# Kernel tuning notes

Measured on AMD Instinct MI355X. Metric: run time of the kernel, lower is better.

## Reference

```python
import jax, jax.numpy as jnp
import numpy as np
from jax.scipy.special import logsumexp

NODES = 128
K = 8
N = 4096  # num data samples; must equal M (original code stacks (N,) with (M,))
Z = NODES * (NODES - 1) // 2


def setup_inputs() -> dict:
    key = jax.random.key(0)
    k1, k2, k3 = jax.random.split(key, 3)
    X = jax.random.normal(k1, (N, NODES), dtype=jnp.float32)
    noise = jax.random.normal(k2, (N, NODES), dtype=jnp.float32)
    theta = jax.random.normal(k3, (K, 2, Z), dtype=jnp.float32)
    logc = jnp.zeros((K,), dtype=jnp.float32)
    return {"X": X, "noise": noise, "theta": theta, "logc": logc}


def reference(X, noise, theta, logc):
    n = X.shape[0]
    m = noise.shape[0]
    nodes = X.shape[1]
    iu, ju = np.triu_indices(nodes, k=1)  # static pair indices, z = nodes*(nodes-1)//2

    def mixture_logprob(A):
        # A: (S, nodes) -> per-component log prob summed over all node pairs, then
        # logsumexp over the K mixture components with weights logc.
        d = A[:, iu] - A[:, ju]                      # (S, z) pairwise phase diffs
        lp = (jnp.einsum('kz,sz->ks', theta[:, 0], jnp.cos(d))
              + jnp.einsum('kz,sz->ks', theta[:, 1], jnp.sin(d)))  # (K, S)
        return logsumexp(lp + logc[:, None], axis=0)  # (S,)

    lp_data = mixture_logprob(X)      # (n,)
    lp_noise = mixture_logprob(noise)  # (m,) == (n,)

    logN = jnp.log(jnp.float32(n))
    logM = jnp.log(jnp.float32(m))
    # log_nx = log_ny = 0 in the original code
    log_J1_denom = jnp.logaddexp(logN + lp_data, logM)
    log_J2_denom = jnp.logaddexp(logN + lp_noise, logM)
    J = (jnp.mean(logN + lp_data - log_J1_denom)
         + jnp.mean(logN - log_J2_denom))
    return J
```

## Files before the change

kernel.cpp:

```cpp
#include <hip/hip_runtime.h>
#include <hip/hip_bf16.h>
#include <math.h>

#define NODES 128
#define KMIX  8
#define NSAMP 4096
#define STOT  8192
#define ZPAIR 8128
#define FDIM  256

using bf16x8 = __attribute__((ext_vector_type(8))) short;
using f32x4  = __attribute__((ext_vector_type(4))) float;

#define OF_F   ((size_t)0)
#define OF_M   (OF_F + (size_t)STOT * FDIM / 2)
#define OF_LP4 (OF_M + (size_t)KMIX * FDIM * FDIM / 2)
#define OF_PT  (OF_LP4 + (size_t)4 * KMIX * STOT)
#define OF_CT  (OF_PT + 32)

#define VMC(N) asm volatile("s_waitcnt vmcnt(" #N ")" ::: "memory")
#define LGKM0  asm volatile("s_waitcnt lgkmcnt(0)" ::: "memory")
#define SBAR   asm volatile("s_barrier" ::: "memory")

__device__ __forceinline__ float bf2f(short u) {
    union { unsigned u32; float f; } cv;
    cv.u32 = ((unsigned)(unsigned short)u) << 16;
    return cv.f;
}
__device__ __forceinline__ short f2bf(float f) {
    union { float f; unsigned u32; } cv; cv.f = f;
    unsigned r = cv.u32 + 0x7fff + ((cv.u32 >> 16) & 1);
    return (short)(r >> 16);
}
__device__ __forceinline__ float softplusf(float x) {
    return fmaxf(x, 0.0f) + log1pf(expf(-fabsf(x)));
}

#define FEAT_BLOCKS (STOT * NODES / 256)
#define WB_BLOCKS   (KMIX * FDIM * FDIM / 256)

__global__ void prep_kernel(const float* __restrict__ X, const float* __restrict__ noise,
                            const float* __restrict__ theta,
                            short* __restrict__ F, short* __restrict__ W,
                            unsigned* __restrict__ ctr) {
    const int b = blockIdx.x, t = threadIdx.x;
    if (b == 0 && t == 0) *ctr = 0u;
    if (b < FEAT_BLOCKS) {
        int idx = b * 256 + t;
        int s = idx >> 7, i = idx & 127;
        float v = (s < NSAMP) ? X[idx] : noise[idx - NSAMP * NODES];
        float sv, cv;
        __sincosf(v, &sv, &cv);
        F[(size_t)s * FDIM + i]       = f2bf(cv);
        F[(size_t)s * FDIM + 128 + i] = f2bf(sv);
    } else {
        int idx = (b - FEAT_BLOCKS) * 256 + t;
        int j = idx & 255, i = (idx >> 8) & 255, k = idx >> 16;
        int a = i & 127, bb = j & 127;
        int hi = i >> 7, hj = j >> 7;
        float val = 0.0f;
        if (a != bb) {
            int p = a < bb ? a : bb;
            int q = a < bb ? bb : a;
            int z = p * 127 - (p * (p - 1)) / 2 + (q - p - 1);
            if (hi == hj) {
                val = 0.5f * theta[(size_t)(k * 2 + 0) * ZPAIR + z];
            } else if (hi == 1 && hj == 0) {
                float t1 = theta[(size_t)(k * 2 + 1) * ZPAIR + z];
                val = (a < bb) ? t1 : -t1;
            }
        }
        W[idx] = f2bf(val);
    }
}

__global__ __launch_bounds__(256, 2) void gemm_fused(
        const short* __restrict__ F, const short* __restrict__ M,
        float* __restrict__ lp2) {
    __shared__ short Ft[2][128 * 64];
    __shared__ short Mt[2][128 * 64];

    const int bid = blockIdx.x;
    const int k   = bid >> 6;
    const int st  = bid & 63;
    const int sbase = st * 128;

    const int t = threadIdx.x;
    const int wid = t >> 6, lane = t & 63;
    const int wm = wid >> 1, wn = wid & 1;

    const short* Mk = M + (size_t)k * FDIM * FDIM;

    const int rg = lane >> 3;
    const int sc = (lane & 7) ^ rg;

    f32x4 acc0[4][4] = {};
    f32x4 acc1[4][4] = {};

    auto stageF = [&](int buf, int c) {
        #pragma unroll
        for (int q = 0; q < 4; q++) {
            int g = wid * 4 + q;
            const short* src = F + ((size_t)(sbase + g * 8 + rg)) * FDIM + c * 64 + sc * 8;
            __builtin_amdgcn_global_load_lds((const unsigned*)src,
                                             (unsigned*)&Ft[buf][g * 512], 16, 0, 0);
        }
    };
    auto stageW = [&](int buf, int ihrow, int c) {
        #pragma unroll
        for (int q = 0; q < 4; q++) {
            int g = wid * 4 + q;
            const short* src = Mk + ((size_t)(ihrow * 128 + g * 8 + rg)) * FDIM + c * 64 + sc * 8;
            __builtin_amdgcn_global_load_lds((const unsigned*)src,
                                             (unsigned*)&Mt[buf][g * 512], 16, 0, 0);
        }
    };

    const int rlow = lane & 15, kq = lane >> 4;

    bf16x8 afr[4][2], bfr[4][2];
    auto loadA = [&](int fbuf) {
        #pragma unroll
        for (int m = 0; m < 4; m++) {
            int row = wm * 64 + m * 16 + rlow;
            #pragma unroll
            for (int kk = 0; kk < 2; kk++) {
                int c16 = (kk * 4 + kq) ^ (row & 7);
                afr[m][kk] = *(const bf16x8*)&Ft[fbuf][row * 64 + c16 * 8];
            }
        }
    };
    auto loadB = [&](int mbuf) {
        #pragma unroll
        for (int n = 0; n < 4; n++) {
            int row = wn * 64 + n * 16 + rlow;
            #pragma unroll
            for (int kk = 0; kk < 2; kk++) {
                int c16 = (kk * 4 + kq) ^ (row & 7);
                bfr[n][kk] = *(const bf16x8*)&Mt[mbuf][row * 64 + c16 * 8];
            }
        }
    };
    auto mfma = [&](f32x4 (&acc)[4][4]) {
        #pragma unroll
        for (int m = 0; m < 4; m++)
            #pragma unroll
            for (int n = 0; n < 4; n++)
                #pragma unroll
                for (int kk = 0; kk < 2; kk++)
                    acc[m][n] = __builtin_amdgcn_mfma_f32_16x16x32_bf16(
                        afr[m][kk], bfr[n][kk], acc[m][n], 0, 0, 0);
    };

    stageF(0, 0); stageW(0, 0, 0); stageW(1, 1, 0);

    VMC(4); SBAR;
    loadA(0); loadB(0);
    LGKM0; SBAR;
    stageF(1, 1); stageW(0, 0, 1);
    mfma(acc0);
    VMC(8); SBAR;
    loadA(0); loadB(1);
    LGKM0; SBAR;
    stageW(1, 1, 1);
    mfma(acc1);
    VMC(4); SBAR;
    loadA(1); loadB(0);
    LGKM0; SBAR;
    stageF(0, 2); stageW(0, 1, 2);
    mfma(acc0);
    VMC(8); SBAR;
    loadA(1); loadB(1);
    LGKM0; SBAR;
    stageF(1, 3); stageW(1, 1, 3);
    mfma(acc1);
    VMC(8); SBAR;
    loadA(0); loadB(0);
    mfma(acc1);
    VMC(0); SBAR;
    loadA(1); loadB(1);
    mfma(acc1);

    float psum[4][4];
    #pragma unroll
    for (int m = 0; m < 4; m++) {
        #pragma unroll
        for (int q = 0; q < 4; q++) {
            int srow = wm * 64 + m * 16 + kq * 4 + q;
            const short* fr0 = F + (size_t)(sbase + srow) * FDIM + wn * 64 + rlow;
            float p = 0.0f;
            #pragma unroll
            for (int n = 0; n < 4; n++)
                p += bf2f(fr0[n * 16]) * acc0[m][n][q];
            #pragma unroll
            for (int n = 0; n < 4; n++)
                p += bf2f(fr0[128 + n * 16]) * acc1[m][n][q];
            psum[m][q] = p;
        }
    }
    #pragma unroll
    for (int off = 1; off < 16; off <<= 1)
        #pragma unroll
        for (int m = 0; m < 4; m++)
            #pragma unroll
            for (int q = 0; q < 4; q++)
                psum[m][q] += __shfl_xor(psum[m][q], off, 64);

    if (rlow == 0) {
        #pragma unroll
        for (int m = 0; m < 4; m++)
            #pragma unroll
            for (int q = 0; q < 4; q++) {
                int srow = wm * 64 + m * 16 + kq * 4 + q;
                lp2[((size_t)wn * KMIX + k) * STOT + sbase + srow] = psum[m][q];
            }
    }
}

__global__ void reduce_kernel(const float* __restrict__ lp2,
                              const float* __restrict__ logc,
                              float* __restrict__ partials,
                              unsigned* __restrict__ counter,
                              float* __restrict__ out) {
    const int t = threadIdx.x;
    const int s = blockIdx.x * 256 + t;

    float v[KMIX];
    #pragma unroll
    for (int k = 0; k < KMIX; k++) {
        v[k] = lp2[((size_t)0 * KMIX + k) * STOT + s]
             + lp2[((size_t)1 * KMIX + k) * STOT + s]
             + logc[k];
    }
    float mx = v[0];
    #pragma unroll
    for (int k = 1; k < KMIX; k++) mx = fmaxf(mx, v[k]);
    float sum = 0.0f;
    #pragma unroll
    for (int k = 0; k < KMIX; k++) sum += expf(v[k] - mx);
    const float lp = mx + logf(sum);

    const float term = (s < NSAMP) ? -softplusf(-lp) : -softplusf(lp);

    float bsum = term;
    #pragma unroll
    for (int off = 32; off; off >>= 1) bsum += __shfl_down(bsum, off);
    __shared__ float wsum[4];
    if ((t & 63) == 0) wsum[t >> 6] = bsum;
    __syncthreads();

    if (t == 0) {
        partials[blockIdx.x] = wsum[0] + wsum[1] + wsum[2] + wsum[3];
        __threadfence();
        unsigned old = atomicAdd(counter, 1u);
        if (old == 31u) {
            __threadfence();
            float tot = 0.0f;
            #pragma unroll
            for (int b = 0; b < 32; b++) tot += partials[b];
            out[0] = tot * (1.0f / (float)NSAMP);
        }
    }
}

extern "C" void kernel_launch(void* const* d_in, const int* in_sizes, int n_in,
                              void* d_out, int out_size, void* d_ws, size_t ws_size,
                              hipStream_t stream) {
    (void)in_sizes; (void)n_in; (void)out_size; (void)ws_size;
    const float* X     = (const float*)d_in[0];
    const float* noise = (const float*)d_in[1];
    const float* theta = (const float*)d_in[2];
    const float* logc  = (const float*)d_in[3];
    float* out = (float*)d_out;
    float* ws  = (float*)d_ws;

    short*    Fb    = (short*)(ws + OF_F);
    short*    Wb    = (short*)(ws + OF_M);
    float*    lp2   = ws + OF_LP4;
    float*    parts = ws + OF_PT;
    unsigned* ctr   = (unsigned*)(ws + OF_CT);

    prep_kernel<<<FEAT_BLOCKS + WB_BLOCKS, 256, 0, stream>>>(X, noise, theta, Fb, Wb, ctr);
    gemm_fused<<<KMIX * (STOT / 128), 256, 0, stream>>>(Fb, Wb, lp2);
    reduce_kernel<<<STOT / 256, 256, 0, stream>>>(lp2, logc, parts, ctr, out);
}
```

Baseline: 26.53 us.

## Vectorize feature prep, transpose lp partials layout, raise MFMA wave priority

The feature prep now handles four elements per thread, using 128-bit loads and 64-bit bf16 stores, which cuts the feature-block count by a factor of four. The per-sample partial log-probs are now stored sample-major, 16 floats per sample, so the reduce kernel reads them with four vector loads instead of 16 strided scalar loads. The GEMM's MFMA loop is wrapped in s_setprio to favour matrix-issuing waves. The gemm's stores to lp16 become scattered, with stride-16 float writes per lane, which may cost more on the write side.

```diff
diff --git a/kernel.cpp b/kernel.cpp
--- a/kernel.cpp
+++ b/kernel.cpp
@@ -14,8 +14,8 @@
 
 #define OF_F   ((size_t)0)
 #define OF_M   (OF_F + (size_t)STOT * FDIM / 2)
-#define OF_LP4 (OF_M + (size_t)KMIX * FDIM * FDIM / 2)
-#define OF_PT  (OF_LP4 + (size_t)4 * KMIX * STOT)
+#define OF_LP  (OF_M + (size_t)KMIX * FDIM * FDIM / 2)
+#define OF_PT  (OF_LP + (size_t)16 * STOT)
 #define OF_CT  (OF_PT + 32)
 
 #define VMC(N) asm volatile("s_waitcnt vmcnt(" #N ")" ::: "memory")
@@ -36,8 +36,8 @@
     return fmaxf(x, 0.0f) + log1pf(expf(-fabsf(x)));
 }
 
-#define FEAT_BLOCKS (STOT * NODES / 256)
-#define WB_BLOCKS   (KMIX * FDIM * FDIM / 256)
+#define FEAT_BLOCKS4 (STOT * NODES / 4 / 256)
+#define WB_BLOCKS    (KMIX * FDIM * FDIM / 256)
 
 __global__ void prep_kernel(const float* __restrict__ X, const float* __restrict__ noise,
                             const float* __restrict__ theta,
@@ -45,16 +45,22 @@
                             unsigned* __restrict__ ctr) {
     const int b = blockIdx.x, t = threadIdx.x;
     if (b == 0 && t == 0) *ctr = 0u;
-    if (b < FEAT_BLOCKS) {
-        int idx = b * 256 + t;
-        int s = idx >> 7, i = idx & 127;
-        float v = (s < NSAMP) ? X[idx] : noise[idx - NSAMP * NODES];
-        float sv, cv;
-        __sincosf(v, &sv, &cv);
-        F[(size_t)s * FDIM + i]       = f2bf(cv);
-        F[(size_t)s * FDIM + 128 + i] = f2bf(sv);
+    if (b < FEAT_BLOCKS4) {
+        int idx4 = (b * 256 + t) * 4;
+        int s = idx4 >> 7, i = idx4 & 127;
+        const float* src = (s < NSAMP) ? (X + idx4) : (noise + (idx4 - NSAMP * NODES));
+        f32x4 v = *(const f32x4*)src;
+        short cb[4], sb[4];
+        #pragma unroll
+        for (int q = 0; q < 4; q++) {
+            float sv, cv;
+            __sincosf(v[q], &sv, &cv);
+            cb[q] = f2bf(cv); sb[q] = f2bf(sv);
+        }
+        *(short4*)&F[(size_t)s * FDIM + i]       = *(short4*)cb;
+        *(short4*)&F[(size_t)s * FDIM + 128 + i] = *(short4*)sb;
     } else {
-        int idx = (b - FEAT_BLOCKS) * 256 + t;
+        int idx = (b - FEAT_BLOCKS4) * 256 + t;
         int j = idx & 255, i = (idx >> 8) & 255, k = idx >> 16;
         int a = i & 127, bb = j & 127;
         int hi = i >> 7, hj = j >> 7;
@@ -76,7 +82,7 @@
 
 __global__ __launch_bounds__(256, 2) void gemm_fused(
         const short* __restrict__ F, const short* __restrict__ M,
-        float* __restrict__ lp2) {
+        float* __restrict__ lp16) {
     __shared__ short Ft[2][128 * 64];
     __shared__ short Mt[2][128 * 64];
 
@@ -142,6 +148,7 @@
         }
     };
     auto mfma = [&](f32x4 (&acc)[4][4]) {
+        __builtin_amdgcn_s_setprio(1);
         #pragma unroll
         for (int m = 0; m < 4; m++)
             #pragma unroll
@@ -150,6 +157,7 @@
                 for (int kk = 0; kk < 2; kk++)
                     acc[m][n] = __builtin_amdgcn_mfma_f32_16x16x32_bf16(
                         afr[m][kk], bfr[n][kk], acc[m][n], 0, 0, 0);
+        __builtin_amdgcn_s_setprio(0);
     };
 
     stageF(0, 0); stageW(0, 0, 0); stageW(1, 1, 0);
@@ -212,12 +220,12 @@
             #pragma unroll
             for (int q = 0; q < 4; q++) {
                 int srow = wm * 64 + m * 16 + kq * 4 + q;
-                lp2[((size_t)wn * KMIX + k) * STOT + sbase + srow] = psum[m][q];
+                lp16[(size_t)(sbase + srow) * 16 + k * 2 + wn] = psum[m][q];
             }
     }
 }
 
-__global__ void reduce_kernel(const float* __restrict__ lp2,
+__global__ void reduce_kernel(const float* __restrict__ lp16,
                               const float* __restrict__ logc,
                               float* __restrict__ partials,
                               unsigned* __restrict__ counter,
@@ -225,13 +233,19 @@
     const int t = threadIdx.x;
     const int s = blockIdx.x * 256 + t;
 
+    const f32x4* base = (const f32x4*)&lp16[(size_t)s * 16];
+    f32x4 r0 = base[0], r1 = base[1], r2 = base[2], r3 = base[3];
+
     float v[KMIX];
-    #pragma unroll
-    for (int k = 0; k < KMIX; k++) {
-        v[k] = lp2[((size_t)0 * KMIX + k) * STOT + s]
-             + lp2[((size_t)1 * KMIX + k) * STOT + s]
-             + logc[k];
-    }
+    v[0] = r0[0] + r0[1] + logc[0];
+    v[1] = r0[2] + r0[3] + logc[1];
+    v[2] = r1[0] + r1[1] + logc[2];
+    v[3] = r1[2] + r1[3] + logc[3];
+    v[4] = r2[0] + r2[1] + logc[4];
+    v[5] = r2[2] + r2[3] + logc[5];
+    v[6] = r3[0] + r3[1] + logc[6];
+    v[7] = r3[2] + r3[3] + logc[7];
+
     float mx = v[0];
     #pragma unroll
     for (int k = 1; k < KMIX; k++) mx = fmaxf(mx, v[k]);
@@ -276,11 +290,11 @@
 
     short*    Fb    = (short*)(ws + OF_F);
     short*    Wb    = (short*)(ws + OF_M);
-    float*    lp2   = ws + OF_LP4;
+    float*    lp16  = ws + OF_LP;
     float*    parts = ws + OF_PT;
     unsigned* ctr   = (unsigned*)(ws + OF_CT);
 
-    prep_kernel<<<FEAT_BLOCKS + WB_BLOCKS, 256, 0, stream>>>(X, noise, theta, Fb, Wb, ctr);
-    gemm_fused<<<KMIX * (STOT / 128), 256, 0, stream>>>(Fb, Wb, lp2);
-    reduce_kernel<<<STOT / 256, 256, 0, stream>>>(lp2, logc, parts, ctr, out);
-}
+    prep_kernel<<<FEAT_BLOCKS4 + WB_BLOCKS, 256, 0, stream>>>(X, noise, theta, Fb, Wb, ctr);
+    gemm_fused<<<KMIX * (STOT / 128), 256, 0, stream>>>(Fb, Wb, lp16);
+    reduce_kernel<<<STOT / 256, 256, 0, stream>>>(lp16, logc, parts, ctr, out);
+}
```

Result: faster. 24.52 us (median of 2 runs) (-7.6%).
